# Optimization experiments

Hardware: AMD Instinct MI355X
Metric: run time of the kernel (lower is better)

## Reference

```python
import jax, jax.numpy as jnp
import numpy as np

LN_EPS = 1e-5  # torch LayerNorm default
EPS = 1e-8     # slot-attention eps

def _ln(x, g, b):
    m = jnp.mean(x, axis=-1, keepdims=True)
    v = jnp.mean(jnp.square(x - m), axis=-1, keepdims=True)
    return (x - m) * jax.lax.rsqrt(v + LN_EPS) * g + b

def setup_inputs() -> dict:
    key = jax.random.key(0)
    ks = jax.random.split(key, 16)
    b, d, n_s, h = 131072, 256, 16, 256
    w_scale = d ** -0.5
    return {
        "inputs": jax.random.normal(ks[0], (b, 1, d), jnp.float32),
        "noise": jax.random.normal(ks[1], (n_s, d), jnp.float32),
        "slots_mu": jax.random.normal(ks[2], (1, d), jnp.float32),
        "slots_sigma": jax.random.uniform(ks[3], (1, d), jnp.float32),
        "Wq": jax.random.normal(ks[4], (d, d), jnp.float32) * w_scale,
        "bq": jnp.zeros((d,), jnp.float32),
        "Wk": jax.random.normal(ks[5], (d, d), jnp.float32) * w_scale,
        "bk": jnp.zeros((d,), jnp.float32),
        "Wv": jax.random.normal(ks[6], (d, d), jnp.float32) * w_scale,
        "bv": jnp.zeros((d,), jnp.float32),
        "W_ih": jax.random.normal(ks[7], (3 * d, d), jnp.float32) * w_scale,
        "W_hh": jax.random.normal(ks[8], (3 * d, d), jnp.float32) * w_scale,
        "b_ih": jnp.zeros((3 * d,), jnp.float32),
        "b_hh": jnp.zeros((3 * d,), jnp.float32),
        "W1": jax.random.normal(ks[9], (h, d), jnp.float32) * w_scale,
        "b1": jnp.zeros((h,), jnp.float32),
        "W2": jax.random.normal(ks[10], (d, h), jnp.float32) * (h ** -0.5),
        "b2": jnp.zeros((d,), jnp.float32),
        "g_in": jnp.ones((d,), jnp.float32),
        "be_in": jnp.zeros((d,), jnp.float32),
        "g_s": jnp.ones((d,), jnp.float32),
        "be_s": jnp.zeros((d,), jnp.float32),
        "g_f": jnp.ones((d,), jnp.float32),
        "be_f": jnp.zeros((d,), jnp.float32),
    }

def reference(inputs, noise, slots_mu, slots_sigma, Wq, bq, Wk, bk, Wv, bv,
              W_ih, W_hh, b_ih, b_hh, W1, b1, W2, b2,
              g_in, be_in, g_s, be_s, g_f, be_f):
    b, w, d = inputs.shape  # w == 1 required by the module's LayerNorm(dim)
    x = inputs.reshape(b, w * d)
    scale = d ** -0.5
    iters = 3

    slots = slots_mu + slots_sigma * noise  # (n_s, d), reparameterized normal

    x = _ln(x, g_in, be_in)
    k = x @ Wk.T + bk  # (b, d)
    v = x @ Wv.T + bv  # (b, d)

    for _ in range(iters):
        slots_prev = slots
        s = _ln(slots, g_s, be_s)
        q = s @ Wq.T + bq                      # (n_s, d)
        dots = jnp.einsum('nd,bd->nb', q, k) * scale
        attn = jax.nn.softmax(dots, axis=0) + EPS   # softmax over slots
        attn = attn / jnp.sum(attn, axis=-1, keepdims=True)
        updates = jnp.einsum('bd,nb->nd', v, attn)  # (n_s, d)
        # torch GRUCell
        gx = updates @ W_ih.T + b_ih                # (n_s, 3d)
        gh = slots_prev @ W_hh.T + b_hh
        xr, xz, xn = jnp.split(gx, 3, axis=-1)
        hr, hz, hn = jnp.split(gh, 3, axis=-1)
        r = jax.nn.sigmoid(xr + hr)
        z = jax.nn.sigmoid(xz + hz)
        n = jnp.tanh(xn + r * hn)
        slots = (1.0 - z) * n + z * slots_prev
        ff = jax.nn.relu(_ln(slots, g_f, be_f) @ W1.T + b1) @ W2.T + b2
        slots = slots + ff
    return slots
```

## Files before the change

### kernel.cpp

```cpp
#include <hip/hip_runtime.h>
#include <stdint.h>

#define B_ROWS 131072
#define SCALE 0.0625f
#define LN_EPS 1e-5f
#define ATTN_EPS 1e-8f

#define BIG_BLOCKS 512
#define BIG_THREADS 512
#define ROWS_PER_BLOCK (B_ROWS / BIG_BLOCKS)
#define ROWS_PER_WAVE  (ROWS_PER_BLOCK / 8)
#define NSLICE BIG_BLOCKS

#define WS_PARTU 0
#define WS_PARTS (WS_PARTU + NSLICE*4096)
#define WS_U     (WS_PARTS + NSLICE*16)
#define WS_S     (WS_U + 4096)
#define WS_SLOTS (WS_S + 64)
#define WS_MID   (WS_SLOTS + 4096)
#define WS_GX    (WS_MID + 4096)
#define WS_GH    (WS_GX + 12288)
#define WS_H1    (WS_GH + 12288)
#define WS_QKG   (WS_H1 + 4096)
#define WS_QB    (WS_QKG + 4096)
#define WS_WIHV  (WS_QB + 64)
#define WS_BGX   (WS_WIHV + 196608)
#define WS_WQKG  (WS_BGX + 768)
#define WS_U2G   (WS_WQKG + 65536)
#define WS_U1    (WS_U2G + 256)
#define WS_C1    (WS_U1 + 256)

__device__ __forceinline__ float dot16(const float* __restrict__ w, const float* s)
{
  float4 w0 = *(const float4*)(w);
  float4 w1 = *(const float4*)(w + 4);
  float4 w2 = *(const float4*)(w + 8);
  float4 w3 = *(const float4*)(w + 12);
  float4 s0 = *(const float4*)(s);
  float4 s1 = *(const float4*)(s + 4);
  float4 s2 = *(const float4*)(s + 8);
  float4 s3 = *(const float4*)(s + 12);
  float a = 0.f;
  a = fmaf(w0.x, s0.x, a); a = fmaf(w0.y, s0.y, a);
  a = fmaf(w0.z, s0.z, a); a = fmaf(w0.w, s0.w, a);
  a = fmaf(w1.x, s1.x, a); a = fmaf(w1.y, s1.y, a);
  a = fmaf(w1.z, s1.z, a); a = fmaf(w1.w, s1.w, a);
  a = fmaf(w2.x, s2.x, a); a = fmaf(w2.y, s2.y, a);
  a = fmaf(w2.z, s2.z, a); a = fmaf(w2.w, s2.w, a);
  a = fmaf(w3.x, s3.x, a); a = fmaf(w3.y, s3.y, a);
  a = fmaf(w3.z, s3.z, a); a = fmaf(w3.w, s3.w, a);
  return a;
}

__global__ __launch_bounds__(256) void k_pre1(
    const float* __restrict__ Wq, const float* __restrict__ bq,
    const float* __restrict__ Wk, const float* __restrict__ bk,
    const float* __restrict__ Wv, const float* __restrict__ bv,
    const float* __restrict__ W_ih, const float* __restrict__ b_ih,
    const float* __restrict__ g_in, const float* __restrict__ be_in,
    float* __restrict__ ws)
{
  int bid = blockIdx.x, t = threadIdx.x;
  int wave = t >> 6, lane = t & 63;
  if (bid < 192) {
    __shared__ __align__(16) float sW[4 * 256];
    __shared__ __align__(16) float sBv[256];
    int j0 = bid * 4;
#pragma unroll
    for (int r = 0; r < 4; r++) sW[r * 256 + t] = W_ih[(j0 + r) * 256 + t];
    sBv[t] = bv[t];
    __syncthreads();
    int d = t;
    float a0 = 0.f, a1 = 0.f, a2 = 0.f, a3 = 0.f;
#pragma unroll 8
    for (int dd = 0; dd < 256; dd++) {
      float v = Wv[dd * 256 + d];
      a0 = fmaf(sW[0 * 256 + dd], v, a0);
      a1 = fmaf(sW[1 * 256 + dd], v, a1);
      a2 = fmaf(sW[2 * 256 + dd], v, a2);
      a3 = fmaf(sW[3 * 256 + dd], v, a3);
    }
    ws[WS_WIHV + (j0 + 0) * 256 + d] = a0;
    ws[WS_WIHV + (j0 + 1) * 256 + d] = a1;
    ws[WS_WIHV + (j0 + 2) * 256 + d] = a2;
    ws[WS_WIHV + (j0 + 3) * 256 + d] = a3;
    float s = 0.f;
#pragma unroll
    for (int q = 0; q < 4; q++) {
      int idx = lane * 4 + q;
      s = fmaf(sW[wave * 256 + idx], sBv[idx], s);
    }
#pragma unroll
    for (int m = 1; m <= 32; m <<= 1) s += __shfl_xor(s, m);
    if (lane == 0) ws[WS_BGX + j0 + wave] = b_ih[j0 + wave] + s;
  } else if (bid < 256) {
    __shared__ __align__(16) float sKc[4 * 256];
    __shared__ __align__(16) float sBq[256];
    int c0 = (bid - 192) * 4;
#pragma unroll
    for (int r = 0; r < 4; r++) sKc[r * 256 + t] = Wk[t * 256 + c0 + r];
    sBq[t] = bq[t];
    __syncthreads();
    int d = t;
    float a0 = 0.f, a1 = 0.f, a2 = 0.f, a3 = 0.f;
#pragma unroll 8
    for (int i = 0; i < 256; i++) {
      float wq = Wq[i * 256 + d];
      a0 = fmaf(wq, sKc[0 * 256 + i], a0);
      a1 = fmaf(wq, sKc[1 * 256 + i], a1);
      a2 = fmaf(wq, sKc[2 * 256 + i], a2);
      a3 = fmaf(wq, sKc[3 * 256 + i], a3);
    }
    ws[WS_WQKG + (c0 + 0) * 256 + d] = SCALE * g_in[c0 + 0] * a0;
    ws[WS_WQKG + (c0 + 1) * 256 + d] = SCALE * g_in[c0 + 1] * a1;
    ws[WS_WQKG + (c0 + 2) * 256 + d] = SCALE * g_in[c0 + 2] * a2;
    ws[WS_WQKG + (c0 + 3) * 256 + d] = SCALE * g_in[c0 + 3] * a3;
    float s = 0.f;
#pragma unroll
    for (int q = 0; q < 4; q++) {
      int idx = lane * 4 + q;
      s = fmaf(sBq[idx], sKc[wave * 256 + idx], s);
    }
#pragma unroll
    for (int m = 1; m <= 32; m <<= 1) s += __shfl_xor(s, m);
    if (lane == 0) ws[WS_U2G + c0 + wave] = SCALE * g_in[c0 + wave] * s;
  } else {
    __shared__ __align__(16) float sBe[256];
    __shared__ __align__(16) float sT2[256];
    sBe[t] = be_in[t];
    __syncthreads();
    float a = 0.f;
#pragma unroll 8
    for (int dp = 0; dp < 256; dp += 4) {
      float4 w = *(const float4*)(Wk + t * 256 + dp);
      a = fmaf(w.x, sBe[dp], fmaf(w.y, sBe[dp + 1],
          fmaf(w.z, sBe[dp + 2], fmaf(w.w, sBe[dp + 3], a))));
    }
    sT2[t] = a + bk[t];
    __syncthreads();
    float u = 0.f;
#pragma unroll 8
    for (int i = 0; i < 256; i++)
      u = fmaf(Wq[i * 256 + t], sT2[i], u);
    ws[WS_U1 + t] = u;
    if (wave == 0) {
      float s = 0.f;
#pragma unroll
      for (int q = 0; q < 4; q++) {
        int idx = lane * 4 + q;
        s = fmaf(bq[idx], sT2[idx], s);
      }
#pragma unroll
      for (int m = 1; m <= 32; m <<= 1) s += __shfl_xor(s, m);
      if (lane == 0) ws[WS_C1] = s;
    }
  }
}

__global__ __launch_bounds__(256) void k_qkg(
    const float* __restrict__ noise, const float* __restrict__ mu,
    const float* __restrict__ sigma, const float* __restrict__ g_s,
    const float* __restrict__ be_s, float* __restrict__ ws, int init)
{
  __shared__ __align__(16) float sS[16 * 260];
  __shared__ __align__(16) float sAux[512];
  __shared__ __align__(16) float sStat[32];
  int bid = blockIdx.x, t = threadIdx.x;
  for (int n = 0; n < 16; n++) {
    float v;
    if (init) v = fmaf(sigma[t], noise[n * 256 + t], mu[t]);
    else      v = ws[WS_SLOTS + n * 256 + t];
    sS[n * 260 + t] = v;
    if (init && bid == 0) ws[WS_SLOTS + n * 256 + t] = v;
  }
  __syncthreads();
  { int n = t >> 4, c = t & 15;
    float s1 = 0.f, s2 = 0.f;
    for (int k = 0; k < 16; k++) {
      float x = sS[n * 260 + c * 16 + k];
      s1 += x; s2 = fmaf(x, x, s2);
    }
    sAux[n * 16 + c] = s1; sAux[256 + n * 16 + c] = s2; }
  __syncthreads();
  if (t < 16) {
    float s1 = 0.f, s2 = 0.f;
    for (int c = 0; c < 16; c++) { s1 += sAux[t * 16 + c]; s2 += sAux[256 + t * 16 + c]; }
    float m = s1 * (1.f / 256.f);
    float v = fmaxf(fmaf(-m, m, s2 * (1.f / 256.f)), 0.f);
    sStat[t] = m; sStat[16 + t] = rsqrtf(v + LN_EPS);
  }
  __syncthreads();
  { float gs = g_s[t], bs = be_s[t];
    for (int n = 0; n < 16; n++) {
      float m = sStat[n], rs = sStat[16 + n];
      sS[n * 260 + t] = fmaf((sS[n * 260 + t] - m) * rs, gs, bs);
    } }
  __syncthreads();
  if (bid < 64) {
    int cr = t >> 6, n = (t >> 2) & 15, ks = t & 3;
    int c = bid * 4 + cr;
    const float* wrow = ws + WS_WQKG + c * 256 + ks * 64;
    const float* srow = &sS[n * 260 + ks * 64];
    float acc = 0.f;
#pragma unroll
    for (int i = 0; i < 16; i++) {
      float4 w = *(const float4*)(wrow + i * 4);
      float4 s4 = *(const float4*)(srow + i * 4);
      acc = fmaf(w.x, s4.x, fmaf(w.y, s4.y, fmaf(w.z, s4.z, fmaf(w.w, s4.w, acc))));
    }
    sAux[t] = acc;
    __syncthreads();
    if (t < 64) {
      int cr2 = t >> 4, n2 = t & 15;
      int c2 = bid * 4 + cr2;
      int b = cr2 * 64 + n2 * 4;
      float s = sAux[b] + sAux[b + 1] + sAux[b + 2] + sAux[b + 3];
      ws[WS_QKG + n2 * 256 + c2] = s + ws[WS_U2G + c2];
    }
  } else {
    int n = t >> 4, ks = t & 15;
    float acc = 0.f;
    for (int k = 0; k < 16; k++)
      acc = fmaf(sS[n * 260 + ks * 16 + k], ws[WS_U1 + ks * 16 + k], acc);
    sAux[t] = acc;
    __syncthreads();
    if (t < 16) {
      float s = 0.f;
      for (int k = 0; k < 16; k++) s += sAux[t * 16 + k];
      ws[WS_QB + t] = SCALE * (s + ws[WS_C1]);
    }
  }
}

__global__ __launch_bounds__(512, 2) void k_big(
    const float* __restrict__ X, float* __restrict__ ws)
{
  __shared__ __align__(16) float red[4 * 4096];
  __shared__ __align__(16) float redS[128];
  int t = threadIdx.x;
  int wave = t >> 6, lane = t & 63;
  int p = lane >> 4, g = lane & 15;

  const float* qkg = ws + WS_QKG;
  float qw[4][16];
  float qs[4];
#pragma unroll
  for (int i = 0; i < 4; i++) {
    const float* rp = qkg + (4 * p + i) * 256 + g * 16;
#pragma unroll
    for (int jq = 0; jq < 4; jq++) {
      float4 v4 = *(const float4*)(rp + 4 * jq);
      qw[i][4 * jq + 0] = v4.x; qw[i][4 * jq + 1] = v4.y;
      qw[i][4 * jq + 2] = v4.z; qw[i][4 * jq + 3] = v4.w;
    }
    float s = 0.f;
#pragma unroll
    for (int j = 0; j < 16; j++) s += qw[i][j];
    qs[i] = s;
  }
#pragma unroll
  for (int m = 1; m <= 8; m <<= 1) {
#pragma unroll
    for (int i = 0; i < 4; i++) qs[i] += __shfl_xor(qs[i], m);
  }
  float qb0[4];
  {
    float4 q4 = *(const float4*)(ws + WS_QB + 4 * p);
    qb0[0] = q4.x; qb0[1] = q4.y; qb0[2] = q4.z; qb0[3] = q4.w;
  }

  float P[4][16];
#pragma unroll
  for (int i = 0; i < 4; i++)
#pragma unroll
    for (int j = 0; j < 16; j++) P[i][j] = 0.f;
  float Q[4] = {0.f, 0.f, 0.f, 0.f};
  float Sa[4] = {0.f, 0.f, 0.f, 0.f};

  size_t rowbase = (size_t)blockIdx.x * ROWS_PER_BLOCK + (size_t)wave * ROWS_PER_WAVE;
  const float* base = X + rowbase * 256 + g * 16;

  float4 cA0 = *(const float4*)(base + 0);
  float4 cB0 = *(const float4*)(base + 4);
  float4 cC0 = *(const float4*)(base + 8);
  float4 cD0 = *(const float4*)(base + 12);
  float4 cA1 = *(const float4*)(base + 256);
  float4 cB1 = *(const float4*)(base + 260);
  float4 cC1 = *(const float4*)(base + 264);
  float4 cD1 = *(const float4*)(base + 268);

#pragma unroll 1
  for (int r = 0; r < ROWS_PER_WAVE; r += 2) {
    const float* nx = base + (size_t)((r + 2 < ROWS_PER_WAVE) ? (r + 2) : 0) * 256;
    float4 pA0 = *(const float4*)(nx + 0);
    float4 pB0 = *(const float4*)(nx + 4);
    float4 pC0 = *(const float4*)(nx + 8);
    float4 pD0 = *(const float4*)(nx + 12);
    float4 pA1 = *(const float4*)(nx + 256);
    float4 pB1 = *(const float4*)(nx + 260);
    float4 pC1 = *(const float4*)(nx + 264);
    float4 pD1 = *(const float4*)(nx + 268);

    float x0[16], x1[16];
    x0[0] = cA0.x; x0[1] = cA0.y; x0[2] = cA0.z; x0[3] = cA0.w;
    x0[4] = cB0.x; x0[5] = cB0.y; x0[6] = cB0.z; x0[7] = cB0.w;
    x0[8] = cC0.x; x0[9] = cC0.y; x0[10] = cC0.z; x0[11] = cC0.w;
    x0[12] = cD0.x; x0[13] = cD0.y; x0[14] = cD0.z; x0[15] = cD0.w;
    x1[0] = cA1.x; x1[1] = cA1.y; x1[2] = cA1.z; x1[3] = cA1.w;
    x1[4] = cB1.x; x1[5] = cB1.y; x1[6] = cB1.z; x1[7] = cB1.w;
    x1[8] = cC1.x; x1[9] = cC1.y; x1[10] = cC1.z; x1[11] = cC1.w;
    x1[12] = cD1.x; x1[13] = cD1.y; x1[14] = cD1.z; x1[15] = cD1.w;

    float s10 = 0.f, s20 = 0.f, s11 = 0.f, s21 = 0.f;
#pragma unroll
    for (int j = 0; j < 16; j++) {
      s10 += x0[j]; s20 = fmaf(x0[j], x0[j], s20);
      s11 += x1[j]; s21 = fmaf(x1[j], x1[j], s21);
    }
#pragma unroll
    for (int m = 1; m <= 8; m <<= 1) {
      s10 += __shfl_xor(s10, m); s11 += __shfl_xor(s11, m);
      s20 += __shfl_xor(s20, m); s21 += __shfl_xor(s21, m);
    }
    float mean0 = s10 * (1.f / 256.f), mean1 = s11 * (1.f / 256.f);
    float var0 = fmaxf(fmaf(-mean0, mean0, s20 * (1.f / 256.f)), 0.f);
    float var1 = fmaxf(fmaf(-mean1, mean1, s21 * (1.f / 256.f)), 0.f);
    float rs0 = rsqrtf(var0 + LN_EPS), rs1 = rsqrtf(var1 + LN_EPS);
    float mrs0 = mean0 * rs0, mrs1 = mean1 * rs1;

    float d0[4] = {0.f, 0.f, 0.f, 0.f};
    float d1[4] = {0.f, 0.f, 0.f, 0.f};
#pragma unroll
    for (int j = 0; j < 16; j++) {
#pragma unroll
      for (int i = 0; i < 4; i++) {
        d0[i] = fmaf(qw[i][j], x0[j], d0[i]);
        d1[i] = fmaf(qw[i][j], x1[j], d1[i]);
      }
    }
#pragma unroll
    for (int m = 1; m <= 8; m <<= 1) {
#pragma unroll
      for (int i = 0; i < 4; i++) {
        d0[i] += __shfl_xor(d0[i], m);
        d1[i] += __shfl_xor(d1[i], m);
      }
    }
    float dsc0[4], dsc1[4];
#pragma unroll
    for (int i = 0; i < 4; i++) {
      dsc0[i] = fmaf(rs0, d0[i], fmaf(-mrs0, qs[i], qb0[i]));
      dsc1[i] = fmaf(rs1, d1[i], fmaf(-mrs1, qs[i], qb0[i]));
    }

    float mx0 = fmaxf(fmaxf(dsc0[0], dsc0[1]), fmaxf(dsc0[2], dsc0[3]));
    float mx1 = fmaxf(fmaxf(dsc1[0], dsc1[1]), fmaxf(dsc1[2], dsc1[3]));
    mx0 = fmaxf(mx0, __shfl_xor(mx0, 16)); mx1 = fmaxf(mx1, __shfl_xor(mx1, 16));
    mx0 = fmaxf(mx0, __shfl_xor(mx0, 32)); mx1 = fmaxf(mx1, __shfl_xor(mx1, 32));
    float e0[4], e1[4];
#pragma unroll
    for (int i = 0; i < 4; i++) {
      e0[i] = __expf(dsc0[i] - mx0);
      e1[i] = __expf(dsc1[i] - mx1);
    }
    float se0 = e0[0] + e0[1] + e0[2] + e0[3];
    float se1 = e1[0] + e1[1] + e1[2] + e1[3];
    se0 += __shfl_xor(se0, 16); se1 += __shfl_xor(se1, 16);
    se0 += __shfl_xor(se0, 32); se1 += __shfl_xor(se1, 32);
    float inv0 = 1.0f / se0, inv1 = 1.0f / se1;
    float a0v[4], ar0[4], a1v[4], ar1[4];
#pragma unroll
    for (int i = 0; i < 4; i++) {
      a0v[i] = fmaf(e0[i], inv0, ATTN_EPS); ar0[i] = a0v[i] * rs0;
      a1v[i] = fmaf(e1[i], inv1, ATTN_EPS); ar1[i] = a1v[i] * rs1;
    }

#pragma unroll
    for (int j = 0; j < 16; j++) {
#pragma unroll
      for (int i = 0; i < 4; i++) {
        P[i][j] = fmaf(ar0[i], x0[j], P[i][j]);
        P[i][j] = fmaf(ar1[i], x1[j], P[i][j]);
      }
    }
#pragma unroll
    for (int i = 0; i < 4; i++) {
      Q[i] = fmaf(a0v[i], mrs0, Q[i]);
      Q[i] = fmaf(a1v[i], mrs1, Q[i]);
      Sa[i] += a0v[i];
      Sa[i] += a1v[i];
    }

    cA0 = pA0; cB0 = pB0; cC0 = pC0; cD0 = pD0;
    cA1 = pA1; cB1 = pB1; cC1 = pC1; cD1 = pD1;
  }

  int slot = wave & 3;
  if (wave < 4) {
#pragma unroll
    for (int i = 0; i < 4; i++) {
#pragma unroll
      for (int jq = 0; jq < 4; jq++) {
        float4 v4;
        v4.x = P[i][4 * jq + 0] - Q[i]; v4.y = P[i][4 * jq + 1] - Q[i];
        v4.z = P[i][4 * jq + 2] - Q[i]; v4.w = P[i][4 * jq + 3] - Q[i];
        *(float4*)&red[slot * 4096 + (4 * p + i) * 256 + g * 16 + jq * 4] = v4;
      }
    }
  }
  if (g == 0) {
#pragma unroll
    for (int i = 0; i < 4; i++) redS[wave * 16 + 4 * p + i] = Sa[i];
  }
  __syncthreads();
  if (wave >= 4) {
#pragma unroll
    for (int i = 0; i < 4; i++) {
#pragma unroll
      for (int jq = 0; jq < 4; jq++) {
        float4* dst = (float4*)&red[slot * 4096 + (4 * p + i) * 256 + g * 16 + jq * 4];
        float4 c = *dst;
        c.x += P[i][4 * jq + 0] - Q[i]; c.y += P[i][4 * jq + 1] - Q[i];
        c.z += P[i][4 * jq + 2] - Q[i]; c.w += P[i][4 * jq + 3] - Q[i];
        *dst = c;
      }
    }
  }
  __syncthreads();
#pragma unroll
  for (int k = 0; k < 8; k++) {
    int idx = k * 512 + t;
    float v = red[idx] + red[4096 + idx] + red[8192 + idx] + red[12288 + idx];
    ws[WS_PARTU + (size_t)blockIdx.x * 4096 + idx] = v;
  }
  if (t < 16) {
    float sv = 0.f;
#pragma unroll
    for (int w = 0; w < 8; w++) sv += redS[w * 16 + t];
    ws[WS_PARTS + blockIdx.x * 16 + t] = sv;
  }
}

__global__ __launch_bounds__(512) void k_slot2(
    const float* __restrict__ W_hh, const float* __restrict__ b_hh,
    const float* __restrict__ g_in, const float* __restrict__ be_in,
    const float* __restrict__ W1, const float* __restrict__ b1,
    const float* __restrict__ g_f, const float* __restrict__ be_f,
    const float* __restrict__ W2, const float* __restrict__ b2v,
    const float* __restrict__ g_s, const float* __restrict__ be_s,
    float* __restrict__ out, float* __restrict__ ws, int last)
{
  __shared__ __align__(16) float sUpd[256];
  __shared__ __align__(16) float sSp[256];
  __shared__ __align__(16) float sGX[768];
  __shared__ __align__(16) float sGH[768];
  __shared__ __align__(16) float sMid[256];
  __shared__ __align__(16) float sVec[256];
  __shared__ __align__(16) float sH1[256];
  __shared__ __align__(16) float sNew[256];
  __shared__ __align__(16) float sR[16];
  __shared__ __align__(16) float sT[512];
  int n = blockIdx.x, t = threadIdx.x;
  int wv = t >> 6, lane = t & 63;
  int j4 = t >> 4, kt = t & 15;
  int tt = t & 255, th = t >> 8;

  {
    float u = 0.f;
    const float* pu = ws + WS_PARTU + (size_t)th * 256 * 4096 + n * 256 + tt;
#pragma unroll 16
    for (int s = 0; s < 256; s++) u += pu[(size_t)s * 4096];
    sT[t] = u;
    float sa = ws[WS_PARTS + t * 16 + n];
#pragma unroll
    for (int m = 1; m <= 32; m <<= 1) sa += __shfl_xor(sa, m);
    if (lane == 0) sR[wv] = sa;
  }
  __syncthreads();
  {
    float S = sR[0] + sR[1] + sR[2] + sR[3] + sR[4] + sR[5] + sR[6] + sR[7];
    float invS = 1.0f / S;
    if (t < 256) {
      float uu = sT[t] + sT[256 + t];
      sUpd[t] = fmaf(g_in[t] * uu, invS, be_in[t]);
      sSp[t] = ws[WS_SLOTS + n * 256 + t];
    }
  }
  __syncthreads();

#pragma unroll 2
  for (int pass = 0; pass < 24; pass++) {
    int j = pass * 32 + j4;
    float a = dot16(ws + WS_WIHV + (size_t)j * 256 + kt * 16, sUpd + kt * 16);
    a += __shfl_xor(a, 1); a += __shfl_xor(a, 2);
    a += __shfl_xor(a, 4); a += __shfl_xor(a, 8);
    if (kt == 0) sGX[j] = a + ws[WS_BGX + j];
  }
#pragma unroll 2
  for (int pass = 0; pass < 24; pass++) {
    int j = pass * 32 + j4;
    float a = dot16(W_hh + (size_t)j * 256 + kt * 16, sSp + kt * 16);
    a += __shfl_xor(a, 1); a += __shfl_xor(a, 2);
    a += __shfl_xor(a, 4); a += __shfl_xor(a, 8);
    if (kt == 0) sGH[j] = a + b_hh[j];
  }
  __syncthreads();

  float mid = 0.f;
  if (t < 256) {
    float xr = sGX[t], xz = sGX[256 + t], xn = sGX[512 + t];
    float hr = sGH[t], hz = sGH[256 + t], hn = sGH[512 + t];
    float sp = sSp[t];
    float r = 1.f / (1.f + __expf(-(xr + hr)));
    float z = 1.f / (1.f + __expf(-(xz + hz)));
    float nn = tanhf(fmaf(r, hn, xn));
    mid = fmaf(z, sp - nn, nn);
    sMid[t] = mid;
  }
  {
    float s1 = mid, s2 = mid * mid;
#pragma unroll
    for (int m = 1; m <= 32; m <<= 1) {
      s1 += __shfl_xor(s1, m); s2 += __shfl_xor(s2, m);
    }
    if (lane == 0) { sR[wv] = s1; sR[8 + wv] = s2; }
  }
  __syncthreads();
  {
    float s1 = sR[0] + sR[1] + sR[2] + sR[3] + sR[4] + sR[5] + sR[6] + sR[7];
    float s2 = sR[8] + sR[9] + sR[10] + sR[11] + sR[12] + sR[13] + sR[14] + sR[15];
    float mean = s1 * (1.f / 256.f);
    float var = fmaxf(fmaf(-mean, mean, s2 * (1.f / 256.f)), 0.f);
    float rs = rsqrtf(var + LN_EPS);
    if (t < 256)
      sVec[t] = fmaf((sMid[t] - mean) * rs, g_f[t], be_f[t]);
  }
  __syncthreads();

#pragma unroll 2
  for (int pass = 0; pass < 8; pass++) {
    int j = pass * 32 + j4;
    float a = dot16(W1 + (size_t)j * 256 + kt * 16, sVec + kt * 16);
    a += __shfl_xor(a, 1); a += __shfl_xor(a, 2);
    a += __shfl_xor(a, 4); a += __shfl_xor(a, 8);
    if (kt == 0) sH1[j] = fmaxf(a + b1[j], 0.f);
  }
  __syncthreads();

#pragma unroll 2
  for (int pass = 0; pass < 8; pass++) {
    int d = pass * 32 + j4;
    float a = dot16(W2 + (size_t)d * 256 + kt * 16, sH1 + kt * 16);
    a += __shfl_xor(a, 1); a += __shfl_xor(a, 2);
    a += __shfl_xor(a, 4); a += __shfl_xor(a, 8);
    if (kt == 0) sNew[d] = a + b2v[d] + sMid[d];
  }
  __syncthreads();
  if (t < 256) {
    float v = sNew[t];
    ws[WS_SLOTS + n * 256 + t] = v;
    out[n * 256 + t] = v;
  }
  if (last) return;

  {
    float v = (t < 256) ? sNew[t] : 0.f;
    float s1 = v, s2 = v * v;
#pragma unroll
    for (int m = 1; m <= 32; m <<= 1) {
      s1 += __shfl_xor(s1, m); s2 += __shfl_xor(s2, m);
    }
    if (lane == 0) { sR[wv] = s1; sR[8 + wv] = s2; }
  }
  __syncthreads();
  {
    float s1 = sR[0] + sR[1] + sR[2] + sR[3] + sR[4] + sR[5] + sR[6] + sR[7];
    float s2 = sR[8] + sR[9] + sR[10] + sR[11] + sR[12] + sR[13] + sR[14] + sR[15];
    float mean = s1 * (1.f / 256.f);
    float var = fmaxf(fmaf(-mean, mean, s2 * (1.f / 256.f)), 0.f);
    float rs = rsqrtf(var + LN_EPS);
    if (t < 256)
      sVec[t] = fmaf((sNew[t] - mean) * rs, g_s[t], be_s[t]);
  }
  __syncthreads();
#pragma unroll 2
  for (int pass = 0; pass < 8; pass++) {
    int c = pass * 32 + j4;
    float a = dot16(ws + WS_WQKG + (size_t)c * 256 + kt * 16, sVec + kt * 16);
    a += __shfl_xor(a, 1); a += __shfl_xor(a, 2);
    a += __shfl_xor(a, 4); a += __shfl_xor(a, 8);
    if (kt == 0) ws[WS_QKG + n * 256 + c] = a + ws[WS_U2G + c];
  }
  {
    float pq = (t < 256) ? sVec[t] * ws[WS_U1 + t] : 0.f;
#pragma unroll
    for (int m = 1; m <= 32; m <<= 1) pq += __shfl_xor(pq, m);
    if (lane == 0) sR[wv] = pq;
  }
  __syncthreads();
  if (t == 0) {
    float s = sR[0] + sR[1] + sR[2] + sR[3] + sR[4] + sR[5] + sR[6] + sR[7];
    ws[WS_QB + n] = SCALE * (s + ws[WS_C1]);
  }
}

extern "C" void kernel_launch(void* const* d_in, const int* in_sizes, int n_in,
                              void* d_out, int out_size, void* d_ws, size_t ws_size,
                              hipStream_t stream)
{
  (void)in_sizes; (void)n_in; (void)out_size; (void)ws_size;
  const float* inputs = (const float*)d_in[0];
  const float* noise  = (const float*)d_in[1];
  const float* mu     = (const float*)d_in[2];
  const float* sigma  = (const float*)d_in[3];
  const float* Wq     = (const float*)d_in[4];
  const float* bq     = (const float*)d_in[5];
  const float* Wk     = (const float*)d_in[6];
  const float* bk     = (const float*)d_in[7];
  const float* Wv     = (const float*)d_in[8];
  const float* bv     = (const float*)d_in[9];
  const float* W_ih   = (const float*)d_in[10];
  const float* W_hh   = (const float*)d_in[11];
  const float* b_ih   = (const float*)d_in[12];
  const float* b_hh   = (const float*)d_in[13];
  const float* W1     = (const float*)d_in[14];
  const float* b1     = (const float*)d_in[15];
  const float* W2     = (const float*)d_in[16];
  const float* b2     = (const float*)d_in[17];
  const float* g_in   = (const float*)d_in[18];
  const float* be_in  = (const float*)d_in[19];
  const float* g_s    = (const float*)d_in[20];
  const float* be_s   = (const float*)d_in[21];
  const float* g_f    = (const float*)d_in[22];
  const float* be_f   = (const float*)d_in[23];
  float* ws = (float*)d_ws;
  float* out = (float*)d_out;

  hipLaunchKernelGGL(k_pre1, dim3(257), dim3(256), 0, stream,
                     Wq, bq, Wk, bk, Wv, bv, W_ih, b_ih, g_in, be_in, ws);
  hipLaunchKernelGGL(k_qkg, dim3(65), dim3(256), 0, stream,
                     noise, mu, sigma, g_s, be_s, ws, 1);
  for (int it = 0; it < 3; it++) {
    hipLaunchKernelGGL(k_big, dim3(BIG_BLOCKS), dim3(BIG_THREADS), 0, stream, inputs, ws);
    hipLaunchKernelGGL(k_slot2, dim3(16), dim3(512), 0, stream,
                       W_hh, b_hh, g_in, be_in, W1, b1, g_f, be_f,
                       W2, b2, g_s, be_s, out, ws, (it == 2) ? 1 : 0);
  }
}
```

Before: 665.5 us.

## Reduce partial updates into 64 slices via atomics and widen slot kernel to 1024 threads

The big kernel now atomically accumulates its per-block partial slot updates into 64 slices instead of writing 512 separate partial buffers. This cuts the serial 256-deep reduction the 16-block slot kernel had to do to 16 loads per thread. The slot kernel now runs 1024 threads and zeroes the slice buffers for the next iteration, and the pre kernel zeroes them for the first. The cost is atomic contention from 8 blocks per slice and nondeterministic float summation order.

```diff
diff --git a/kernel.cpp b/kernel.cpp
--- a/kernel.cpp
+++ b/kernel.cpp
@@ -10,11 +10,11 @@
 #define BIG_THREADS 512
 #define ROWS_PER_BLOCK (B_ROWS / BIG_BLOCKS)
 #define ROWS_PER_WAVE  (ROWS_PER_BLOCK / 8)
-#define NSLICE BIG_BLOCKS
+#define NSLICE 64
 
 #define WS_PARTU 0
-#define WS_PARTS (WS_PARTU + NSLICE*4096)
-#define WS_U     (WS_PARTS + NSLICE*16)
+#define WS_PARTS (WS_PARTU + 512*4096)
+#define WS_U     (WS_PARTS + 512*16)
 #define WS_S     (WS_U + 4096)
 #define WS_SLOTS (WS_S + 64)
 #define WS_MID   (WS_SLOTS + 4096)
@@ -62,6 +62,15 @@
 {
   int bid = blockIdx.x, t = threadIdx.x;
   int wave = t >> 6, lane = t & 63;
+  if (bid < 256) {
+#pragma unroll
+    for (int q = 0; q < 4; q++)
+      ws[WS_PARTU + bid * 1024 + q * 256 + t] = 0.f;
+  } else {
+#pragma unroll
+    for (int q = 0; q < 4; q++)
+      ws[WS_PARTS + q * 256 + t] = 0.f;
+  }
   if (bid < 192) {
     __shared__ __align__(16) float sW[4 * 256];
     __shared__ __align__(16) float sBv[256];
@@ -427,21 +436,22 @@
     }
   }
   __syncthreads();
+  int slice = blockIdx.x & 63;
 #pragma unroll
   for (int k = 0; k < 8; k++) {
     int idx = k * 512 + t;
     float v = red[idx] + red[4096 + idx] + red[8192 + idx] + red[12288 + idx];
-    ws[WS_PARTU + (size_t)blockIdx.x * 4096 + idx] = v;
+    atomicAdd(&ws[WS_PARTU + (size_t)slice * 4096 + idx], v);
   }
   if (t < 16) {
     float sv = 0.f;
 #pragma unroll
     for (int w = 0; w < 8; w++) sv += redS[w * 16 + t];
-    ws[WS_PARTS + blockIdx.x * 16 + t] = sv;
+    atomicAdd(&ws[WS_PARTS + slice * 16 + t], sv);
   }
 }
 
-__global__ __launch_bounds__(512) void k_slot2(
+__global__ __launch_bounds__(1024) void k_slot3(
     const float* __restrict__ W_hh, const float* __restrict__ b_hh,
     const float* __restrict__ g_in, const float* __restrict__ be_in,
     const float* __restrict__ W1, const float* __restrict__ b1,
@@ -450,6 +460,7 @@
     const float* __restrict__ g_s, const float* __restrict__ be_s,
     float* __restrict__ out, float* __restrict__ ws, int last)
 {
+  __shared__ __align__(16) float sT[1024];
   __shared__ __align__(16) float sUpd[256];
   __shared__ __align__(16) float sSp[256];
   __shared__ __align__(16) float sGX[768];
@@ -458,47 +469,54 @@
   __shared__ __align__(16) float sVec[256];
   __shared__ __align__(16) float sH1[256];
   __shared__ __align__(16) float sNew[256];
-  __shared__ __align__(16) float sR[16];
-  __shared__ __align__(16) float sT[512];
+  __shared__ __align__(16) float sR[32];
   int n = blockIdx.x, t = threadIdx.x;
   int wv = t >> 6, lane = t & 63;
-  int j4 = t >> 4, kt = t & 15;
-  int tt = t & 255, th = t >> 8;
-
-  {
+  int j16 = t >> 4, kt = t & 15;
+  int tt = t & 255, sg = t >> 8;
+
+  {
+    const float* pu = ws + WS_PARTU + (size_t)(sg * 16) * 4096 + n * 256 + tt;
     float u = 0.f;
-    const float* pu = ws + WS_PARTU + (size_t)th * 256 * 4096 + n * 256 + tt;
-#pragma unroll 16
-    for (int s = 0; s < 256; s++) u += pu[(size_t)s * 4096];
+#pragma unroll
+    for (int s = 0; s < 16; s++) u += pu[(size_t)s * 4096];
     sT[t] = u;
-    float sa = ws[WS_PARTS + t * 16 + n];
-#pragma unroll
-    for (int m = 1; m <= 32; m <<= 1) sa += __shfl_xor(sa, m);
-    if (lane == 0) sR[wv] = sa;
-  }
-  __syncthreads();
-  {
-    float S = sR[0] + sR[1] + sR[2] + sR[3] + sR[4] + sR[5] + sR[6] + sR[7];
-    float invS = 1.0f / S;
+    if (wv == 0) {
+      float sa = ws[WS_PARTS + t * 16 + n];
+#pragma unroll
+      for (int m = 1; m <= 32; m <<= 1) sa += __shfl_xor(sa, m);
+      if (lane == 0) sR[0] = sa;
+    }
+  }
+  __syncthreads();
+  {
+    float invS = 1.0f / sR[0];
     if (t < 256) {
-      float uu = sT[t] + sT[256 + t];
+      float uu = sT[t] + sT[256 + t] + sT[512 + t] + sT[768 + t];
       sUpd[t] = fmaf(g_in[t] * uu, invS, be_in[t]);
       sSp[t] = ws[WS_SLOTS + n * 256 + t];
     }
   }
   __syncthreads();
 
+  if (!last) {
+#pragma unroll
+    for (int i = 0; i < 16; i++)
+      ws[WS_PARTU + (size_t)i * 16384 + n * 1024 + t] = 0.f;
+    if (n == 0) ws[WS_PARTS + t] = 0.f;
+  }
+
 #pragma unroll 2
-  for (int pass = 0; pass < 24; pass++) {
-    int j = pass * 32 + j4;
+  for (int pass = 0; pass < 12; pass++) {
+    int j = pass * 64 + j16;
     float a = dot16(ws + WS_WIHV + (size_t)j * 256 + kt * 16, sUpd + kt * 16);
     a += __shfl_xor(a, 1); a += __shfl_xor(a, 2);
     a += __shfl_xor(a, 4); a += __shfl_xor(a, 8);
     if (kt == 0) sGX[j] = a + ws[WS_BGX + j];
   }
 #pragma unroll 2
-  for (int pass = 0; pass < 24; pass++) {
-    int j = pass * 32 + j4;
+  for (int pass = 0; pass < 12; pass++) {
+    int j = pass * 64 + j16;
     float a = dot16(W_hh + (size_t)j * 256 + kt * 16, sSp + kt * 16);
     a += __shfl_xor(a, 1); a += __shfl_xor(a, 2);
     a += __shfl_xor(a, 4); a += __shfl_xor(a, 8);
@@ -523,12 +541,13 @@
     for (int m = 1; m <= 32; m <<= 1) {
       s1 += __shfl_xor(s1, m); s2 += __shfl_xor(s2, m);
     }
-    if (lane == 0) { sR[wv] = s1; sR[8 + wv] = s2; }
-  }
-  __syncthreads();
-  {
-    float s1 = sR[0] + sR[1] + sR[2] + sR[3] + sR[4] + sR[5] + sR[6] + sR[7];
-    float s2 = sR[8] + sR[9] + sR[10] + sR[11] + sR[12] + sR[13] + sR[14] + sR[15];
+    if (lane == 0) { sR[wv] = s1; sR[16 + wv] = s2; }
+  }
+  __syncthreads();
+  {
+    float s1 = 0.f, s2 = 0.f;
+#pragma unroll
+    for (int w = 0; w < 16; w++) { s1 += sR[w]; s2 += sR[16 + w]; }
     float mean = s1 * (1.f / 256.f);
     float var = fmaxf(fmaf(-mean, mean, s2 * (1.f / 256.f)), 0.f);
     float rs = rsqrtf(var + LN_EPS);
@@ -538,8 +557,8 @@
   __syncthreads();
 
 #pragma unroll 2
-  for (int pass = 0; pass < 8; pass++) {
-    int j = pass * 32 + j4;
+  for (int pass = 0; pass < 4; pass++) {
+    int j = pass * 64 + j16;
     float a = dot16(W1 + (size_t)j * 256 + kt * 16, sVec + kt * 16);
     a += __shfl_xor(a, 1); a += __shfl_xor(a, 2);
     a += __shfl_xor(a, 4); a += __shfl_xor(a, 8);
@@ -548,8 +567,8 @@
   __syncthreads();
 
 #pragma unroll 2
-  for (int pass = 0; pass < 8; pass++) {
-    int d = pass * 32 + j4;
+  for (int pass = 0; pass < 4; pass++) {
+    int d = pass * 64 + j16;
     float a = dot16(W2 + (size_t)d * 256 + kt * 16, sH1 + kt * 16);
     a += __shfl_xor(a, 1); a += __shfl_xor(a, 2);
     a += __shfl_xor(a, 4); a += __shfl_xor(a, 8);
@@ -570,12 +589,13 @@
     for (int m = 1; m <= 32; m <<= 1) {
       s1 += __shfl_xor(s1, m); s2 += __shfl_xor(s2, m);
     }
-    if (lane == 0) { sR[wv] = s1; sR[8 + wv] = s2; }
-  }
-  __syncthreads();
-  {
-    float s1 = sR[0] + sR[1] + sR[2] + sR[3] + sR[4] + sR[5] + sR[6] + sR[7];
-    float s2 = sR[8] + sR[9] + sR[10] + sR[11] + sR[12] + sR[13] + sR[14] + sR[15];
+    if (lane == 0) { sR[wv] = s1; sR[16 + wv] = s2; }
+  }
+  __syncthreads();
+  {
+    float s1 = 0.f, s2 = 0.f;
+#pragma unroll
+    for (int w = 0; w < 16; w++) { s1 += sR[w]; s2 += sR[16 + w]; }
     float mean = s1 * (1.f / 256.f);
     float var = fmaxf(fmaf(-mean, mean, s2 * (1.f / 256.f)), 0.f);
     float rs = rsqrtf(var + LN_EPS);
@@ -584,8 +604,8 @@
   }
   __syncthreads();
 #pragma unroll 2
-  for (int pass = 0; pass < 8; pass++) {
-    int c = pass * 32 + j4;
+  for (int pass = 0; pass < 4; pass++) {
+    int c = pass * 64 + j16;
     float a = dot16(ws + WS_WQKG + (size_t)c * 256 + kt * 16, sVec + kt * 16);
     a += __shfl_xor(a, 1); a += __shfl_xor(a, 2);
     a += __shfl_xor(a, 4); a += __shfl_xor(a, 8);
@@ -599,7 +619,9 @@
   }
   __syncthreads();
   if (t == 0) {
-    float s = sR[0] + sR[1] + sR[2] + sR[3] + sR[4] + sR[5] + sR[6] + sR[7];
+    float s = 0.f;
+#pragma unroll
+    for (int w = 0; w < 16; w++) s += sR[w];
     ws[WS_QB + n] = SCALE * (s + ws[WS_C1]);
   }
 }
@@ -642,7 +664,7 @@
                      noise, mu, sigma, g_s, be_s, ws, 1);
   for (int it = 0; it < 3; it++) {
     hipLaunchKernelGGL(k_big, dim3(BIG_BLOCKS), dim3(BIG_THREADS), 0, stream, inputs, ws);
-    hipLaunchKernelGGL(k_slot2, dim3(16), dim3(512), 0, stream,
+    hipLaunchKernelGGL(k_slot3, dim3(16), dim3(1024), 0, stream,
                        W_hh, b_hh, g_in, be_in, W1, b1, g_f, be_f,
                        W2, b2, g_s, be_s, out, ws, (it == 2) ? 1 : 0);
   }
```

New measurement: 587.5 us. 1.13x faster.

## Reduce partials atomically into 8 slices and split GRU gate matmuls into wide kernel

Applied to the files above, without the earlier changes.

k_big now atomically adds its per-block partial updates into 8 slices instead of writing 512 separate partials, so the slot kernel no longer has to sum 512 partials serially. The GRU input and hidden gate matmuls move out of the 16-block slot kernel into a new 128-block kernel, spreading the 768x256 weight reads across more CUs. The tail kernel zeroes the slices for the next iteration, and the LayerNorm-stat and q-dot loops in k_big are fused. The cost is float atomic contention on 8 slices, nondeterministic summation order, and one extra kernel launch per iteration.

```diff
diff --git a/kernel.cpp b/kernel.cpp
--- a/kernel.cpp
+++ b/kernel.cpp
@@ -10,11 +10,11 @@
 #define BIG_THREADS 512
 #define ROWS_PER_BLOCK (B_ROWS / BIG_BLOCKS)
 #define ROWS_PER_WAVE  (ROWS_PER_BLOCK / 8)
-#define NSLICE BIG_BLOCKS
+#define NSLICE 8
 
 #define WS_PARTU 0
-#define WS_PARTS (WS_PARTU + NSLICE*4096)
-#define WS_U     (WS_PARTS + NSLICE*16)
+#define WS_PARTS (WS_PARTU + 512*4096)
+#define WS_U     (WS_PARTS + 512*16)
 #define WS_S     (WS_U + 4096)
 #define WS_SLOTS (WS_S + 64)
 #define WS_MID   (WS_SLOTS + 4096)
@@ -62,6 +62,13 @@
 {
   int bid = blockIdx.x, t = threadIdx.x;
   int wave = t >> 6, lane = t & 63;
+  if (bid < 32) {
+#pragma unroll
+    for (int q = 0; q < 4; q++)
+      ws[WS_PARTU + bid * 1024 + q * 256 + t] = 0.f;
+  } else if (bid == 256) {
+    if (t < 128) ws[WS_PARTS + t] = 0.f;
+  }
   if (bid < 192) {
     __shared__ __align__(16) float sW[4 * 256];
     __shared__ __align__(16) float sBv[256];
@@ -312,15 +319,27 @@
     x1[12] = cD1.x; x1[13] = cD1.y; x1[14] = cD1.z; x1[15] = cD1.w;
 
     float s10 = 0.f, s20 = 0.f, s11 = 0.f, s21 = 0.f;
+    float d0[4] = {0.f, 0.f, 0.f, 0.f};
+    float d1[4] = {0.f, 0.f, 0.f, 0.f};
 #pragma unroll
     for (int j = 0; j < 16; j++) {
       s10 += x0[j]; s20 = fmaf(x0[j], x0[j], s20);
       s11 += x1[j]; s21 = fmaf(x1[j], x1[j], s21);
+#pragma unroll
+      for (int i = 0; i < 4; i++) {
+        d0[i] = fmaf(qw[i][j], x0[j], d0[i]);
+        d1[i] = fmaf(qw[i][j], x1[j], d1[i]);
+      }
     }
 #pragma unroll
     for (int m = 1; m <= 8; m <<= 1) {
       s10 += __shfl_xor(s10, m); s11 += __shfl_xor(s11, m);
       s20 += __shfl_xor(s20, m); s21 += __shfl_xor(s21, m);
+#pragma unroll
+      for (int i = 0; i < 4; i++) {
+        d0[i] += __shfl_xor(d0[i], m);
+        d1[i] += __shfl_xor(d1[i], m);
+      }
     }
     float mean0 = s10 * (1.f / 256.f), mean1 = s11 * (1.f / 256.f);
     float var0 = fmaxf(fmaf(-mean0, mean0, s20 * (1.f / 256.f)), 0.f);
@@ -328,24 +347,6 @@
     float rs0 = rsqrtf(var0 + LN_EPS), rs1 = rsqrtf(var1 + LN_EPS);
     float mrs0 = mean0 * rs0, mrs1 = mean1 * rs1;
 
-    float d0[4] = {0.f, 0.f, 0.f, 0.f};
-    float d1[4] = {0.f, 0.f, 0.f, 0.f};
-#pragma unroll
-    for (int j = 0; j < 16; j++) {
-#pragma unroll
-      for (int i = 0; i < 4; i++) {
-        d0[i] = fmaf(qw[i][j], x0[j], d0[i]);
-        d1[i] = fmaf(qw[i][j], x1[j], d1[i]);
-      }
-    }
-#pragma unroll
-    for (int m = 1; m <= 8; m <<= 1) {
-#pragma unroll
-      for (int i = 0; i < 4; i++) {
-        d0[i] += __shfl_xor(d0[i], m);
-        d1[i] += __shfl_xor(d1[i], m);
-      }
-    }
     float dsc0[4], dsc1[4];
 #pragma unroll
     for (int i = 0; i < 4; i++) {
@@ -427,96 +428,104 @@
     }
   }
   __syncthreads();
+  int slice = blockIdx.x & 7;
 #pragma unroll
   for (int k = 0; k < 8; k++) {
     int idx = k * 512 + t;
     float v = red[idx] + red[4096 + idx] + red[8192 + idx] + red[12288 + idx];
-    ws[WS_PARTU + (size_t)blockIdx.x * 4096 + idx] = v;
+    atomicAdd(&ws[WS_PARTU + (size_t)slice * 4096 + idx], v);
   }
   if (t < 16) {
     float sv = 0.f;
 #pragma unroll
     for (int w = 0; w < 8; w++) sv += redS[w * 16 + t];
-    ws[WS_PARTS + blockIdx.x * 16 + t] = sv;
+    atomicAdd(&ws[WS_PARTS + slice * 16 + t], sv);
   }
 }
 
-__global__ __launch_bounds__(512) void k_slot2(
+__global__ __launch_bounds__(256) void k_gxgh(
     const float* __restrict__ W_hh, const float* __restrict__ b_hh,
     const float* __restrict__ g_in, const float* __restrict__ be_in,
+    float* __restrict__ ws)
+{
+  __shared__ __align__(16) float sU[16 * 260];
+  __shared__ __align__(16) float sInv[16];
+  int bid = blockIdx.x, t = threadIdx.x;
+  bool isgx = bid < 64;
+  if (isgx && t < 16) {
+    float s = 0.f;
+#pragma unroll
+    for (int sl = 0; sl < NSLICE; sl++) s += ws[WS_PARTS + sl * 16 + t];
+    sInv[t] = 1.0f / s;
+  }
+  __syncthreads();
+  if (isgx) {
+    float gi = g_in[t], bi = be_in[t];
+    for (int n = 0; n < 16; n++) {
+      float acc = 0.f;
+#pragma unroll
+      for (int sl = 0; sl < NSLICE; sl++)
+        acc += ws[WS_PARTU + (size_t)sl * 4096 + n * 256 + t];
+      sU[n * 260 + t] = fmaf(gi * acc, sInv[n], bi);
+    }
+  } else {
+    for (int n = 0; n < 16; n++)
+      sU[n * 260 + t] = ws[WS_SLOTS + n * 256 + t];
+  }
+  __syncthreads();
+  int jr = t >> 4, n = t & 15;
+  if (jr < 12) {
+    int j = (isgx ? bid : bid - 64) * 12 + jr;
+    const float* srow = &sU[n * 260];
+    const float* wrow = isgx ? (ws + WS_WIHV + j * 256) : (W_hh + j * 256);
+    float acc = isgx ? ws[WS_BGX + j] : b_hh[j];
+#pragma unroll 8
+    for (int k = 0; k < 64; k++) {
+      float4 w = *(const float4*)(wrow + k * 4);
+      float4 s4 = *(const float4*)(srow + k * 4);
+      acc = fmaf(w.x, s4.x, fmaf(w.y, s4.y, fmaf(w.z, s4.z, fmaf(w.w, s4.w, acc))));
+    }
+    if (isgx) ws[WS_GX + n * 768 + j] = acc;
+    else      ws[WS_GH + n * 768 + j] = acc;
+  }
+}
+
+__global__ __launch_bounds__(512) void k_tail(
     const float* __restrict__ W1, const float* __restrict__ b1,
     const float* __restrict__ g_f, const float* __restrict__ be_f,
     const float* __restrict__ W2, const float* __restrict__ b2v,
     const float* __restrict__ g_s, const float* __restrict__ be_s,
     float* __restrict__ out, float* __restrict__ ws, int last)
 {
-  __shared__ __align__(16) float sUpd[256];
-  __shared__ __align__(16) float sSp[256];
-  __shared__ __align__(16) float sGX[768];
-  __shared__ __align__(16) float sGH[768];
   __shared__ __align__(16) float sMid[256];
   __shared__ __align__(16) float sVec[256];
   __shared__ __align__(16) float sH1[256];
   __shared__ __align__(16) float sNew[256];
-  __shared__ __align__(16) float sR[16];
-  __shared__ __align__(16) float sT[512];
+  __shared__ __align__(16) float sR[32];
   int n = blockIdx.x, t = threadIdx.x;
   int wv = t >> 6, lane = t & 63;
-  int j4 = t >> 4, kt = t & 15;
-  int tt = t & 255, th = t >> 8;
+  int j16 = t >> 4, kt = t & 15;
 
   {
-    float u = 0.f;
-    const float* pu = ws + WS_PARTU + (size_t)th * 256 * 4096 + n * 256 + tt;
-#pragma unroll 16
-    for (int s = 0; s < 256; s++) u += pu[(size_t)s * 4096];
-    sT[t] = u;
-    float sa = ws[WS_PARTS + t * 16 + n];
-#pragma unroll
-    for (int m = 1; m <= 32; m <<= 1) sa += __shfl_xor(sa, m);
-    if (lane == 0) sR[wv] = sa;
-  }
-  __syncthreads();
-  {
-    float S = sR[0] + sR[1] + sR[2] + sR[3] + sR[4] + sR[5] + sR[6] + sR[7];
-    float invS = 1.0f / S;
-    if (t < 256) {
-      float uu = sT[t] + sT[256 + t];
-      sUpd[t] = fmaf(g_in[t] * uu, invS, be_in[t]);
-      sSp[t] = ws[WS_SLOTS + n * 256 + t];
-    }
-  }
-  __syncthreads();
-
-#pragma unroll 2
-  for (int pass = 0; pass < 24; pass++) {
-    int j = pass * 32 + j4;
-    float a = dot16(ws + WS_WIHV + (size_t)j * 256 + kt * 16, sUpd + kt * 16);
-    a += __shfl_xor(a, 1); a += __shfl_xor(a, 2);
-    a += __shfl_xor(a, 4); a += __shfl_xor(a, 8);
-    if (kt == 0) sGX[j] = a + ws[WS_BGX + j];
-  }
-#pragma unroll 2
-  for (int pass = 0; pass < 24; pass++) {
-    int j = pass * 32 + j4;
-    float a = dot16(W_hh + (size_t)j * 256 + kt * 16, sSp + kt * 16);
-    a += __shfl_xor(a, 1); a += __shfl_xor(a, 2);
-    a += __shfl_xor(a, 4); a += __shfl_xor(a, 8);
-    if (kt == 0) sGH[j] = a + b_hh[j];
-  }
-  __syncthreads();
+    int gid = n * 512 + t;
+    float4 z4 = {0.f, 0.f, 0.f, 0.f};
+    *(float4*)&ws[WS_PARTU + gid * 4] = z4;
+    if (n == 0 && t < 128) ws[WS_PARTS + t] = 0.f;
+  }
 
   float mid = 0.f;
   if (t < 256) {
-    float xr = sGX[t], xz = sGX[256 + t], xn = sGX[512 + t];
-    float hr = sGH[t], hz = sGH[256 + t], hn = sGH[512 + t];
-    float sp = sSp[t];
+    float xr = ws[WS_GX + n * 768 + t],       hr = ws[WS_GH + n * 768 + t];
+    float xz = ws[WS_GX + n * 768 + 256 + t], hz = ws[WS_GH + n * 768 + 256 + t];
+    float xn = ws[WS_GX + n * 768 + 512 + t], hn = ws[WS_GH + n * 768 + 512 + t];
+    float sp = ws[WS_SLOTS + n * 256 + t];
     float r = 1.f / (1.f + __expf(-(xr + hr)));
     float z = 1.f / (1.f + __expf(-(xz + hz)));
     float nn = tanhf(fmaf(r, hn, xn));
     mid = fmaf(z, sp - nn, nn);
     sMid[t] = mid;
   }
+
   {
     float s1 = mid, s2 = mid * mid;
 #pragma unroll
@@ -539,7 +548,7 @@
 
 #pragma unroll 2
   for (int pass = 0; pass < 8; pass++) {
-    int j = pass * 32 + j4;
+    int j = pass * 32 + j16;
     float a = dot16(W1 + (size_t)j * 256 + kt * 16, sVec + kt * 16);
     a += __shfl_xor(a, 1); a += __shfl_xor(a, 2);
     a += __shfl_xor(a, 4); a += __shfl_xor(a, 8);
@@ -549,7 +558,7 @@
 
 #pragma unroll 2
   for (int pass = 0; pass < 8; pass++) {
-    int d = pass * 32 + j4;
+    int d = pass * 32 + j16;
     float a = dot16(W2 + (size_t)d * 256 + kt * 16, sH1 + kt * 16);
     a += __shfl_xor(a, 1); a += __shfl_xor(a, 2);
     a += __shfl_xor(a, 4); a += __shfl_xor(a, 8);
@@ -585,7 +594,7 @@
   __syncthreads();
 #pragma unroll 2
   for (int pass = 0; pass < 8; pass++) {
-    int c = pass * 32 + j4;
+    int c = pass * 32 + j16;
     float a = dot16(ws + WS_WQKG + (size_t)c * 256 + kt * 16, sVec + kt * 16);
     a += __shfl_xor(a, 1); a += __shfl_xor(a, 2);
     a += __shfl_xor(a, 4); a += __shfl_xor(a, 8);
@@ -641,9 +650,12 @@
   hipLaunchKernelGGL(k_qkg, dim3(65), dim3(256), 0, stream,
                      noise, mu, sigma, g_s, be_s, ws, 1);
   for (int it = 0; it < 3; it++) {
-    hipLaunchKernelGGL(k_big, dim3(BIG_BLOCKS), dim3(BIG_THREADS), 0, stream, inputs, ws);
-    hipLaunchKernelGGL(k_slot2, dim3(16), dim3(512), 0, stream,
-                       W_hh, b_hh, g_in, be_in, W1, b1, g_f, be_f,
-                       W2, b2, g_s, be_s, out, ws, (it == 2) ? 1 : 0);
+    hipLaunchKernelGGL(k_big, dim3(BIG_BLOCKS), dim3(BIG_THREADS), 0, stream,
+                       inputs, ws);
+    hipLaunchKernelGGL(k_gxgh, dim3(128), dim3(256), 0, stream,
+                       W_hh, b_hh, g_in, be_in, ws);
+    hipLaunchKernelGGL(k_tail, dim3(16), dim3(512), 0, stream,
+                       W1, b1, g_f, be_f, W2, b2, g_s, be_s,
+                       out, ws, (it == 2) ? 1 : 0);
   }
 }
```

New measurement: 549.0 us. 1.21x faster.
